# Performance work log

Measured on AMD Instinct MI355X. Metric: run time of the kernel, lower is better.

The kernel has to match this reference:

```python
import jax, jax.numpy as jnp
import numpy as np

H = 768       # hidden size
NH = 12       # num attention heads
DH = H // NH  # head dim = 64
B = 32
S = 512


def setup_inputs() -> dict:
    key = jax.random.key(0)
    ks = jax.random.split(key, 7)
    scale = 1.0 / np.sqrt(H)
    return {
        "inputs": jax.random.normal(ks[0], (B, S, H), dtype=jnp.float32),
        "Wq": jax.random.normal(ks[1], (H, H), dtype=jnp.float32) * scale,
        "bq": jnp.zeros((H,), dtype=jnp.float32),
        "Wk": jax.random.normal(ks[2], (H, H), dtype=jnp.float32) * scale,
        "bk": jnp.zeros((H,), dtype=jnp.float32),
        "Wv": jax.random.normal(ks[3], (H, H), dtype=jnp.float32) * scale,
        "bv": jnp.zeros((H,), dtype=jnp.float32),
    }


def reference(inputs, Wq, bq, Wk, bk, Wv, bv):
    # BertSelfAttention: linear projections (torch Linear: x @ W.T + b)
    def split_heads(x):  # [B,S,H] -> [B,NH,S,DH]
        return x.reshape(B, S, NH, DH).transpose(0, 2, 1, 3)

    q = split_heads(inputs @ Wq.T + bq)
    k = split_heads(inputs @ Wk.T + bk)
    v = split_heads(inputs @ Wv.T + bv)

    # scores [B,NH,S,S]; the wrapper adds an all-zero attention mask (no-op)
    scores = jnp.einsum("bhqd,bhkd->bhqk", q, k) / jnp.sqrt(jnp.float32(DH))
    probs = jax.nn.softmax(scores, axis=-1)
    ctx = jnp.einsum("bhqk,bhkd->bhqd", probs, v)  # [B,NH,S,DH]
    ctx = ctx.transpose(0, 2, 1, 3).reshape(B, S, H)
    return jnp.tanh(ctx)
```

## Files before the change

### kernel.cpp

```cpp
#include <hip/hip_runtime.h>
#include <hip/hip_bf16.h>
#include <cmath>

#define Bc   32
#define Sc_  512
#define Hc   768
#define NHc  12
#define DHc  64
#define Mc   (Bc * Sc_)
#define Ntot (3 * Hc)

#define QSCALE 0.18033688011112042f

typedef __attribute__((ext_vector_type(8))) short short8v;
typedef __attribute__((ext_vector_type(8))) unsigned short ushort8v;
typedef __attribute__((ext_vector_type(4))) float f32x4;

static __device__ __forceinline__ ushort f2b(float f) {
    __hip_bfloat16 h = __float2bfloat16(f);
    return *reinterpret_cast<ushort*>(&h);
}

static __device__ __forceinline__ void gl2lds(const ushort* g, ushort* l) {
    __builtin_amdgcn_global_load_lds(
        (const __attribute__((address_space(1))) unsigned int*)g,
        (__attribute__((address_space(3))) unsigned int*)l, 16, 0, 0);
}

static __device__ __forceinline__ float fast_tanh(float x) {
    float e = __builtin_amdgcn_exp2f(x * 2.885390081777927f);
    return 1.0f - 2.0f * __builtin_amdgcn_rcpf(e + 1.0f);
}

__global__ __launch_bounds__(256) void convert_pack(
    const float* __restrict__ X,
    const float* __restrict__ Wq, const float* __restrict__ Wk,
    const float* __restrict__ Wv,
    const float* __restrict__ bq, const float* __restrict__ bk,
    const float* __restrict__ bv,
    ushort* __restrict__ Xt, ushort* __restrict__ Wt, float* __restrict__ bbp)
{
    const int bx = blockIdx.x;
    const int t  = threadIdx.x;

    __shared__ ushort T[128 * 36];

    const float* base;
    ushort* out;
    if (bx < 128) {
        base = X + (size_t)bx * 128 * Hc;
        out  = Xt + (size_t)bx * (96 * 1024);
    } else {
        int nblk = bx - 128;
        int n0 = nblk * 128;
        int z = n0 / Hc;
        int nn0 = n0 - z * Hc;
        const float* W = (z == 0) ? Wq : (z == 1) ? Wk : Wv;
        base = W + (size_t)nn0 * Hc;
        out  = Wt + (size_t)nblk * (96 * 1024);
    }

    const int row_r = t >> 1, half = t & 1;
    const int row_w = t & 127, cb = t >> 7;

    for (int pp = 0; pp < 4; ++pp) {
        const int pass = blockIdx.y * 4 + pp;
        const int k0 = pass * 32;
        const float* p = base + (size_t)row_r * Hc + k0 + half * 16;
        float4 f0 = *(const float4*)&p[0];
        float4 f1 = *(const float4*)&p[4];
        float4 f2 = *(const float4*)&p[8];
        float4 f3 = *(const float4*)&p[12];
        int wb = row_r * 36 + half * 16;
        ushort4 u0, u1, u2, u3;
        u0.x = f2b(f0.x); u0.y = f2b(f0.y); u0.z = f2b(f0.z); u0.w = f2b(f0.w);
        u1.x = f2b(f1.x); u1.y = f2b(f1.y); u1.z = f2b(f1.z); u1.w = f2b(f1.w);
        u2.x = f2b(f2.x); u2.y = f2b(f2.y); u2.z = f2b(f2.z); u2.w = f2b(f2.w);
        u3.x = f2b(f3.x); u3.y = f2b(f3.y); u3.z = f2b(f3.z); u3.w = f2b(f3.w);
        *(ushort4*)&T[wb + 0]  = u0;
        *(ushort4*)&T[wb + 4]  = u1;
        *(ushort4*)&T[wb + 8]  = u2;
        *(ushort4*)&T[wb + 12] = u3;
        __syncthreads();
        #pragma unroll
        for (int u = 0; u < 2; ++u) {
            int c = cb * 2 + u;
            ushort4 lo = *(const ushort4*)&T[row_w * 36 + c * 8];
            ushort4 hi = *(const ushort4*)&T[row_w * 36 + c * 8 + 4];
            ushort8v v;
            *(ushort4*)&v = lo;
            *((ushort4*)&v + 1) = hi;
            *(ushort8v*)&out[(size_t)(pass * 4 + c) * 1024 + row_w * 8] = v;
        }
        __syncthreads();
    }

    if (bx == 0 && blockIdx.y == 0) {
        for (int i = t; i < Ntot; i += 256) {
            int z = i / Hc, nn = i - z * Hc;
            bbp[i] = ((z == 0) ? bq : (z == 1) ? bk : bv)[nn];
        }
    }
}

__global__ __launch_bounds__(256) void qkv_mfma(
    const ushort* __restrict__ Xt, const ushort* __restrict__ Wt,
    const float* __restrict__ bbp,
    ushort* __restrict__ Qb, ushort* __restrict__ Kt, ushort* __restrict__ Vt)
{
    const int tid = threadIdx.x;
    const int wave = tid >> 6, lane = tid & 63;
    const int quad = lane >> 4, l16 = lane & 15;
    const int wr = wave >> 1, wc = wave & 1;
    const int m0 = blockIdx.x * 128;
    const int n0 = blockIdx.y * 128;

    __shared__ __align__(16) ushort As[4096];
    __shared__ __align__(16) ushort Bs[4096];

    f32x4 acc[4][4];
    #pragma unroll
    for (int i = 0; i < 4; ++i)
        #pragma unroll
        for (int j = 0; j < 4; ++j) acc[i][j] = (f32x4)(0.f);

    const ushort* gA = Xt + (size_t)blockIdx.x * (96 * 1024) + wave * 1024 + lane * 8;
    const ushort* gB = Wt + (size_t)blockIdx.y * (96 * 1024) + wave * 1024 + lane * 8;
    ushort* lA = As + wave * 1024;
    ushort* lB = Bs + wave * 1024;

    for (int t = 0; t < 24; ++t) {
        const ushort* ga = gA + t * 4096;
        const ushort* gb = gB + t * 4096;
        gl2lds(ga,       lA);
        gl2lds(ga + 512, lA + 512);
        gl2lds(gb,       lB);
        gl2lds(gb + 512, lB + 512);
        __syncthreads();

        short8v a[4], b[4];
        #pragma unroll
        for (int i = 0; i < 4; ++i)
            a[i] = *(const short8v*)&As[quad * 1024 + (wr * 64 + i * 16 + l16) * 8];
        #pragma unroll
        for (int j = 0; j < 4; ++j)
            b[j] = *(const short8v*)&Bs[quad * 1024 + (wc * 64 + j * 16 + l16) * 8];
        #pragma unroll
        for (int i = 0; i < 4; ++i)
            #pragma unroll
            for (int j = 0; j < 4; ++j)
                acc[i][j] = __builtin_amdgcn_mfma_f32_16x16x32_bf16(
                    a[i], b[j], acc[i][j], 0, 0, 0);
        __syncthreads();
    }

    const int z = n0 / Hc;
    #pragma unroll
    for (int j = 0; j < 4; ++j) {
        const int n  = n0 + wc * 64 + j * 16 + l16;
        const int nn = n - z * Hc;
        const int h  = nn >> 6, d = nn & 63;
        const float bias = bbp[n];
        #pragma unroll
        for (int i = 0; i < 4; ++i) {
            const int mbase = m0 + wr * 64 + i * 16 + quad * 4;
            const int bb = mbase >> 9;
            const int s0 = mbase & 511;
            const size_t head = (size_t)(bb * NHc + h) * (Sc_ * DHc);
            if (z == 0) {
                size_t base = head + (size_t)s0 * DHc + d;
                #pragma unroll
                for (int r = 0; r < 4; ++r)
                    Qb[base + (size_t)r * DHc] = f2b((acc[i][j][r] + bias) * QSCALE);
            } else if (z == 1) {
                size_t base = head + (s0 >> 6) * 4096 + (d >> 3) * 512
                            + (s0 & 63) * 8 + (d & 7);
                #pragma unroll
                for (int r = 0; r < 4; ++r)
                    Kt[base + r * 8] = f2b(acc[i][j][r] + bias);
            } else {
                size_t base = head + (s0 >> 6) * 4096 + ((s0 & 63) >> 3) * 512
                            + d * 8 + (s0 & 7);
                ushort4 o;
                o.x = f2b(acc[i][j][0] + bias);
                o.y = f2b(acc[i][j][1] + bias);
                o.z = f2b(acc[i][j][2] + bias);
                o.w = f2b(acc[i][j][3] + bias);
                *(ushort4*)&Vt[base] = o;
            }
        }
    }
}

__global__ __launch_bounds__(256) void attn_mfma(
    const ushort* __restrict__ Qb, const ushort* __restrict__ Kt,
    const ushort* __restrict__ Vt, float* __restrict__ out)
{
    const int bid = blockIdx.x;
    const int super = bid >> 5, l = bid & 31;
    const int head_lin = super * 8 + (l & 7);
    const int qt = l >> 3;
    const int b = head_lin / NHc, h = head_lin % NHc;

    const int wave = threadIdx.x >> 6;
    const int lane = threadIdx.x & 63;
    const int quad = lane >> 4, l16 = lane & 15;
    const int q0 = qt * 128 + wave * 32;
    const int sw = l16 & 7;

    const size_t head = (size_t)head_lin * (Sc_ * DHc);
    const ushort* __restrict__ Q = Qb + head;
    const ushort* __restrict__ K = Kt + head;
    const ushort* __restrict__ V = Vt + head;

    __shared__ __align__(16) ushort Plds[4][2][1024];

    short8v aq[2][2];
    #pragma unroll
    for (int u = 0; u < 2; ++u)
        #pragma unroll
        for (int hf = 0; hf < 2; ++hf)
            aq[u][hf] = *(const short8v*)
                &Q[(size_t)(q0 + u * 16 + l16) * DHc + hf * 32 + quad * 8];

    f32x4 o[2][4];
    #pragma unroll
    for (int u = 0; u < 2; ++u)
        #pragma unroll
        for (int t = 0; t < 4; ++t) o[u][t] = (f32x4)(0.f);
    float rs[2] = {0.f, 0.f};

    for (int kb = 0; kb < 8; ++kb) {
        const ushort* Kb_ = K + kb * 4096;
        const ushort* Vb_ = V + kb * 4096;

        short8v kf[4][2];
        #pragma unroll
        for (int t = 0; t < 4; ++t) {
            kf[t][0] = *(const short8v*)&Kb_[quad * 512 + (t * 16 + l16) * 8];
            kf[t][1] = *(const short8v*)&Kb_[(4 + quad) * 512 + (t * 16 + l16) * 8];
        }

        f32x4 sa[2][4];
        #pragma unroll
        for (int u = 0; u < 2; ++u)
            #pragma unroll
            for (int t = 0; t < 4; ++t) {
                f32x4 s = __builtin_amdgcn_mfma_f32_16x16x32_bf16(
                    kf[t][0], aq[u][0], (f32x4)(0.f), 0, 0, 0);
                sa[u][t] = __builtin_amdgcn_mfma_f32_16x16x32_bf16(
                    kf[t][1], aq[u][1], s, 0, 0, 0);
            }

        #pragma unroll
        for (int u = 0; u < 2; ++u) {
            #pragma unroll
            for (int t = 0; t < 4; ++t) {
                float p0 = __builtin_amdgcn_exp2f(sa[u][t][0]);
                float p1 = __builtin_amdgcn_exp2f(sa[u][t][1]);
                float p2 = __builtin_amdgcn_exp2f(sa[u][t][2]);
                float p3 = __builtin_amdgcn_exp2f(sa[u][t][3]);
                rs[u] += (p0 + p1) + (p2 + p3);
                ushort4 pk;
                pk.x = f2b(p0); pk.y = f2b(p1); pk.z = f2b(p2); pk.w = f2b(p3);
                int c = t * 2 + (quad >> 1);
                int addr = l16 * 64 + ((c ^ sw) * 8) + (quad & 1) * 4;
                *(ushort4*)&Plds[wave][u][addr] = pk;
            }
        }

        short8v pa[2][2];
        #pragma unroll
        for (int u = 0; u < 2; ++u) {
            pa[u][0] = *(const short8v*)&Plds[wave][u][l16 * 64 + ((quad ^ sw) * 8)];
            pa[u][1] = *(const short8v*)&Plds[wave][u][l16 * 64 + (((4 + quad) ^ sw) * 8)];
        }

        #pragma unroll
        for (int t2 = 0; t2 < 4; ++t2) {
            short8v vf0 = *(const short8v*)&Vb_[quad * 512 + (t2 * 16 + l16) * 8];
            short8v vf1 = *(const short8v*)&Vb_[(4 + quad) * 512 + (t2 * 16 + l16) * 8];
            #pragma unroll
            for (int u = 0; u < 2; ++u) {
                o[u][t2] = __builtin_amdgcn_mfma_f32_16x16x32_bf16(
                    pa[u][0], vf0, o[u][t2], 0, 0, 0);
                o[u][t2] = __builtin_amdgcn_mfma_f32_16x16x32_bf16(
                    pa[u][1], vf1, o[u][t2], 0, 0, 0);
            }
        }
    }

    #pragma unroll
    for (int u = 0; u < 2; ++u) {
        float l2 = rs[u];
        l2 += __shfl_xor(l2, 16);
        l2 += __shfl_xor(l2, 32);
        #pragma unroll
        for (int r = 0; r < 4; ++r) {
            float lr = __shfl(l2, quad * 4 + r);
            float inv = 1.0f / lr;
            int q = q0 + u * 16 + quad * 4 + r;
            size_t base = ((size_t)b * Sc_ + q) * Hc + h * DHc;
            #pragma unroll
            for (int t2 = 0; t2 < 4; ++t2)
                out[base + t2 * 16 + l16] = fast_tanh(o[u][t2][r] * inv);
        }
    }
}

extern "C" void kernel_launch(void* const* d_in, const int* in_sizes, int n_in,
                              void* d_out, int out_size, void* d_ws, size_t ws_size,
                              hipStream_t stream) {
    const float* X  = (const float*)d_in[0];
    const float* Wq = (const float*)d_in[1];
    const float* bq = (const float*)d_in[2];
    const float* Wk = (const float*)d_in[3];
    const float* bk = (const float*)d_in[4];
    const float* Wv = (const float*)d_in[5];
    const float* bv = (const float*)d_in[6];
    float* out = (float*)d_out;

    ushort* Qb  = (ushort*)d_ws;
    ushort* Kt  = Qb + (size_t)Mc * Hc;
    ushort* Vt  = Kt + (size_t)Mc * Hc;
    ushort* Xt  = Vt + (size_t)Mc * Hc;
    ushort* Wt  = Xt + (size_t)Mc * Hc;
    float*  bbp = (float*)(Wt + (size_t)Ntot * Hc);

    dim3 g0(146, 6);
    convert_pack<<<g0, 256, 0, stream>>>(X, Wq, Wk, Wv, bq, bk, bv, Xt, Wt, bbp);

    dim3 g1(Mc / 128, Ntot / 128);
    qkv_mfma<<<g1, 256, 0, stream>>>(Xt, Wt, bbp, Qb, Kt, Vt);

    attn_mfma<<<dim3(1536), 256, 0, stream>>>(Qb, Kt, Vt, out);
}
```

Baseline: 224.9 us.

## Drop LDS transpose in convert pack and compute softmax row sums via MFMA

The fp32-to-bf16 packing kernel drops its shared-memory staging and barriers. Each thread now reads 8 contiguous floats and writes one packed 16-byte chunk straight to the blocked layout, over a flat 1752-block grid. In attention, the per-lane scalar row sums and their cross-lane shuffle reduction are replaced by extra MFMAs that multiply the bf16 probabilities by a ones vector. This yields row sums already laid out like the output, at the cost of a few more matrix instructions and summing the bf16-rounded probabilities. Paired float-to-bf16 conversion intrinsics are also used.

Result: slower. 230.5 us (+2.4%).

```diff
diff --git a/kernel.cpp b/kernel.cpp
--- a/kernel.cpp
+++ b/kernel.cpp
@@ -19,6 +19,10 @@
 static __device__ __forceinline__ ushort f2b(float f) {
     __hip_bfloat16 h = __float2bfloat16(f);
     return *reinterpret_cast<ushort*>(&h);
+}
+static __device__ __forceinline__ ushort2 f2b2(float a, float b) {
+    __hip_bfloat162 h = __float22bfloat162_rn(float2{a, b});
+    return *reinterpret_cast<ushort2*>(&h);
 }
 
 static __device__ __forceinline__ void gl2lds(const ushort* g, ushort* l) {
@@ -41,17 +45,16 @@
     ushort* __restrict__ Xt, ushort* __restrict__ Wt, float* __restrict__ bbp)
 {
     const int bx = blockIdx.x;
-    const int t  = threadIdx.x;
-
-    __shared__ ushort T[128 * 36];
+    const int panel = bx / 12, kcg = bx % 12;
+    const int t = threadIdx.x;
 
     const float* base;
     ushort* out;
-    if (bx < 128) {
-        base = X + (size_t)bx * 128 * Hc;
-        out  = Xt + (size_t)bx * (96 * 1024);
+    if (panel < 128) {
+        base = X + (size_t)panel * 128 * Hc;
+        out  = Xt + (size_t)panel * (96 * 1024);
     } else {
-        int nblk = bx - 128;
+        int nblk = panel - 128;
         int n0 = nblk * 128;
         int z = n0 / Hc;
         int nn0 = n0 - z * Hc;
@@ -60,42 +63,26 @@
         out  = Wt + (size_t)nblk * (96 * 1024);
     }
 
-    const int row_r = t >> 1, half = t & 1;
-    const int row_w = t & 127, cb = t >> 7;
-
-    for (int pp = 0; pp < 4; ++pp) {
-        const int pass = blockIdx.y * 4 + pp;
-        const int k0 = pass * 32;
-        const float* p = base + (size_t)row_r * Hc + k0 + half * 16;
+    #pragma unroll
+    for (int v = 0; v < 4; ++v) {
+        int idx  = v * 256 + t;
+        int row  = idx & 127;
+        int kc_l = idx >> 7;
+        int kc   = kcg * 8 + kc_l;
+        const float* p = base + (size_t)row * Hc + kc * 8;
         float4 f0 = *(const float4*)&p[0];
         float4 f1 = *(const float4*)&p[4];
-        float4 f2 = *(const float4*)&p[8];
-        float4 f3 = *(const float4*)&p[12];
-        int wb = row_r * 36 + half * 16;
-        ushort4 u0, u1, u2, u3;
-        u0.x = f2b(f0.x); u0.y = f2b(f0.y); u0.z = f2b(f0.z); u0.w = f2b(f0.w);
-        u1.x = f2b(f1.x); u1.y = f2b(f1.y); u1.z = f2b(f1.z); u1.w = f2b(f1.w);
-        u2.x = f2b(f2.x); u2.y = f2b(f2.y); u2.z = f2b(f2.z); u2.w = f2b(f2.w);
-        u3.x = f2b(f3.x); u3.y = f2b(f3.y); u3.z = f2b(f3.z); u3.w = f2b(f3.w);
-        *(ushort4*)&T[wb + 0]  = u0;
-        *(ushort4*)&T[wb + 4]  = u1;
-        *(ushort4*)&T[wb + 8]  = u2;
-        *(ushort4*)&T[wb + 12] = u3;
-        __syncthreads();
-        #pragma unroll
-        for (int u = 0; u < 2; ++u) {
-            int c = cb * 2 + u;
-            ushort4 lo = *(const ushort4*)&T[row_w * 36 + c * 8];
-            ushort4 hi = *(const ushort4*)&T[row_w * 36 + c * 8 + 4];
-            ushort8v v;
-            *(ushort4*)&v = lo;
-            *((ushort4*)&v + 1) = hi;
-            *(ushort8v*)&out[(size_t)(pass * 4 + c) * 1024 + row_w * 8] = v;
-        }
-        __syncthreads();
-    }
-
-    if (bx == 0 && blockIdx.y == 0) {
+        ushort2 h0 = f2b2(f0.x, f0.y);
+        ushort2 h1 = f2b2(f0.z, f0.w);
+        ushort2 h2 = f2b2(f1.x, f1.y);
+        ushort2 h3 = f2b2(f1.z, f1.w);
+        ushort8v o;
+        o[0] = h0.x; o[1] = h0.y; o[2] = h1.x; o[3] = h1.y;
+        o[4] = h2.x; o[5] = h2.y; o[6] = h3.x; o[7] = h3.y;
+        *(ushort8v*)&out[(size_t)kc * 1024 + row * 8] = o;
+    }
+
+    if (bx == 0) {
         for (int i = t; i < Ntot; i += 256) {
             int z = i / Hc, nn = i - z * Hc;
             bbp[i] = ((z == 0) ? bq : (z == 1) ? bk : bv)[nn];
@@ -223,12 +210,17 @@
             aq[u][hf] = *(const short8v*)
                 &Q[(size_t)(q0 + u * 16 + l16) * DHc + hf * 32 + quad * 8];
 
-    f32x4 o[2][4];
-    #pragma unroll
-    for (int u = 0; u < 2; ++u)
+    short8v ones;
+    #pragma unroll
+    for (int i = 0; i < 8; ++i) ones[i] = (short)0x3F80;
+
+    f32x4 o[2][4], rsum[2];
+    #pragma unroll
+    for (int u = 0; u < 2; ++u) {
+        rsum[u] = (f32x4)(0.f);
         #pragma unroll
         for (int t = 0; t < 4; ++t) o[u][t] = (f32x4)(0.f);
-    float rs[2] = {0.f, 0.f};
+    }
 
     for (int kb = 0; kb < 8; ++kb) {
         const ushort* Kb_ = K + kb * 4096;
@@ -260,9 +252,10 @@
                 float p1 = __builtin_amdgcn_exp2f(sa[u][t][1]);
                 float p2 = __builtin_amdgcn_exp2f(sa[u][t][2]);
                 float p3 = __builtin_amdgcn_exp2f(sa[u][t][3]);
-                rs[u] += (p0 + p1) + (p2 + p3);
+                ushort2 lo = f2b2(p0, p1);
+                ushort2 hi = f2b2(p2, p3);
                 ushort4 pk;
-                pk.x = f2b(p0); pk.y = f2b(p1); pk.z = f2b(p2); pk.w = f2b(p3);
+                pk.x = lo.x; pk.y = lo.y; pk.z = hi.x; pk.w = hi.y;
                 int c = t * 2 + (quad >> 1);
                 int addr = l16 * 64 + ((c ^ sw) * 8) + (quad & 1) * 4;
                 *(ushort4*)&Plds[wave][u][addr] = pk;
@@ -274,6 +267,14 @@
         for (int u = 0; u < 2; ++u) {
             pa[u][0] = *(const short8v*)&Plds[wave][u][l16 * 64 + ((quad ^ sw) * 8)];
             pa[u][1] = *(const short8v*)&Plds[wave][u][l16 * 64 + (((4 + quad) ^ sw) * 8)];
+        }
+
+        #pragma unroll
+        for (int u = 0; u < 2; ++u) {
+            rsum[u] = __builtin_amdgcn_mfma_f32_16x16x32_bf16(
+                pa[u][0], ones, rsum[u], 0, 0, 0);
+            rsum[u] = __builtin_amdgcn_mfma_f32_16x16x32_bf16(
+                pa[u][1], ones, rsum[u], 0, 0, 0);
         }
 
         #pragma unroll
@@ -292,13 +293,9 @@
 
     #pragma unroll
     for (int u = 0; u < 2; ++u) {
-        float l2 = rs[u];
-        l2 += __shfl_xor(l2, 16);
-        l2 += __shfl_xor(l2, 32);
         #pragma unroll
         for (int r = 0; r < 4; ++r) {
-            float lr = __shfl(l2, quad * 4 + r);
-            float inv = 1.0f / lr;
+            float inv = __builtin_amdgcn_rcpf(rsum[u][r]);
             int q = q0 + u * 16 + quad * 4 + r;
             size_t base = ((size_t)b * Sc_ + q) * Hc + h * DHc;
             #pragma unroll
@@ -327,8 +324,8 @@
     ushort* Wt  = Xt + (size_t)Mc * Hc;
     float*  bbp = (float*)(Wt + (size_t)Ntot * Hc);
 
-    dim3 g0(146, 6);
-    convert_pack<<<g0, 256, 0, stream>>>(X, Wq, Wk, Wv, bq, bk, bv, Xt, Wt, bbp);
+    convert_pack<<<dim3(1752), 256, 0, stream>>>(
+        X, Wq, Wk, Wv, bq, bk, bv, Xt, Wt, bbp);
 
     dim3 g1(Mc / 128, Ntot / 128);
     qkv_mfma<<<g1, 256, 0, stream>>>(Xt, Wt, bbp, Qb, Kt, Vt);
```
